# Kernel optimization log

Measured on AMD Instinct MI355X. Metric: run time of the kernel, lower is better.

The kernel has to match this reference:

```python
import jax, jax.numpy as jnp
import numpy as np

K = 8          # number of nearest neighbors (init kwarg k)
EPS = 1e-16    # torch_geometric clamps squared distance at 1e-16


def setup_inputs() -> dict:
    key = jax.random.key(0)
    k1, k2, k3, k4 = jax.random.split(key, 4)
    N, D, B = 16384, 128, 64
    x1 = jax.random.normal(k1, (N, 3 + D), dtype=jnp.float32)  # true graph: [coords(3) | feats(D)]
    x2 = jax.random.normal(k2, (N, 3 + D), dtype=jnp.float32)  # pred graph
    b1 = jnp.sort(jax.random.randint(k3, (N,), 0, B))          # sorted per-node graph ids
    b2 = jnp.sort(jax.random.randint(k4, (N,), 0, B))
    return {"x1": x1, "x2": x2, "b1": b1, "b2": b2}


def _knn_interpolate(f1, c1, c2, b1, b2, k):
    # Squared pairwise distances [N2, N1] via ||a||^2 + ||b||^2 - 2ab (GEMM form).
    d2 = (jnp.sum(c2 * c2, axis=-1)[:, None]
          + jnp.sum(c1 * c1, axis=-1)[None, :]
          - 2.0 * (c2 @ c1.T))
    d2 = jnp.maximum(d2, 0.0)
    # Batch-aware kNN: forbid cross-graph neighbors.
    d2 = jnp.where(b2[:, None] != b1[None, :], jnp.inf, d2)
    neg_d2, idx = jax.lax.top_k(-d2, k)          # k smallest distances per target node
    w = 1.0 / jnp.clip(-neg_d2, EPS)             # [N2, k] inverse-squared-distance weights
    nbr = f1[idx]                                # [N2, k, D] gather of neighbor features
    return jnp.einsum('nk,nkd->nd', w, nbr) / jnp.sum(w, axis=-1, keepdims=True)


def reference(x1, x2, b1, b2):
    c1, f1 = x1[:, :3], x1[:, 3:]
    c2, f2 = x2[:, :3], x2[:, 3:]
    f1_interp = _knn_interpolate(f1, c1, c2, b1, b2, K)
    return jnp.mean((f1_interp - f2) ** 2)
```

## Files before the change

kernel.cpp:

```cpp
#include <hip/hip_runtime.h>
#include <math.h>

#define KNN 8
#define QPB 32
#define SUB 16
#define BLK 512
#define CAP 1024

__launch_bounds__(BLK, 4)
__global__ void knn_one(const float* __restrict__ x1,
                        const float* __restrict__ x2,
                        const int* __restrict__ b1,
                        const int* __restrict__ b2,
                        int N, int ROW, float scale,
                        unsigned long long* __restrict__ slot,
                        float* __restrict__ out) {
  __shared__ float4 c4[CAP];
  __shared__ int   bs[CAP];
  __shared__ int   s_info[2];
  __shared__ float wred[BLK / 64];

  const int nwg = (int)gridDim.x;
  const int xcd = (int)blockIdx.x & 7, pos = (int)blockIdx.x >> 3;
  const int q8 = nwg >> 3, r8 = nwg & 7;
  const int bid = (xcd < r8) ? xcd * (q8 + 1) + pos
                             : r8 * (q8 + 1) + (xcd - r8) * q8 + pos;

  const int tid  = threadIdx.x;
  const int lane = tid & 63;
  const int wv   = tid >> 6;
  const int qi   = tid >> 4;
  const int sub  = tid & (SUB - 1);
  const int q0   = bid * QPB;
  const int q    = min(q0 + qi, N - 1);
  const int qlast = min(q0 + QPB - 1, N - 1);

  float qx, qy, qz; int mybatch;
  float f2v[KNN];
  {
    const float* c2 = x2 + (size_t)q * ROW;
    qx = c2[0]; qy = c2[1]; qz = c2[2];
    mybatch = b2[q];
    const float* f2 = c2 + 3 + sub;
#pragma unroll
    for (int t = 0; t < KNN; ++t) f2v[t] = f2[16 * t];
  }
  const float n2 = qx * qx + qy * qy + qz * qz;

  if (wv < 2) {
    const int bb = (wv == 0) ? b2[q0] : b2[qlast];
    const int target = bb + wv;
    int lo = 0, hi = N;
    while (lo < hi) {
      int step = (hi - lo + 63) >> 6;
      int p = lo + lane * step;
      bool pred = (p < hi) && (b1[p] < target);
      int c = __popcll(__ballot(pred));
      if (c == 0) { hi = lo; break; }
      int nlo = lo + (c - 1) * step + 1;
      hi = min(hi, lo + c * step);
      lo = nlo;
    }
    if (lane == 0) s_info[wv] = lo;
  }

  float dist[KNN]; int nidx[KNN];
#pragma unroll
  for (int k = 0; k < KNN; ++k) { dist[k] = INFINITY; nidx[k] = 0; }

  __syncthreads();
  const int s1v = s_info[0], e1v = s_info[1];

  for (int t0 = s1v; t0 < e1v; t0 += CAP) {
    const int t1 = min(t0 + CAP, e1v);
    __syncthreads();
    for (int i = t0 + tid; i < t1; i += BLK) {
      const float* p = x1 + (size_t)i * ROW;
      float cx = p[0], cy = p[1], cz = p[2];
      c4[i - t0] = make_float4(cx, cy, cz, cx * cx + cy * cy + cz * cz);
      bs[i - t0] = b1[i];
    }
    __syncthreads();
    for (int j = t0 + sub; j < t1; j += SUB) {
      float4 c = c4[j - t0];
      int bv = bs[j - t0];
      float d = fmaxf(fmaf(-2.0f, fmaf(qx, c.x, fmaf(qy, c.y, qz * c.z)), n2 + c.w), 0.0f);
      d = (bv == mybatch) ? d : INFINITY;
      bool lt[KNN];
#pragma unroll
      for (int k = 0; k < KNN; ++k) lt[k] = d < dist[k];
#pragma unroll
      for (int k = KNN - 1; k > 0; --k) {
        dist[k] = lt[k - 1] ? dist[k - 1] : (lt[k] ? d : dist[k]);
        nidx[k] = lt[k - 1] ? nidx[k - 1] : (lt[k] ? j : nidx[k]);
      }
      dist[0] = lt[0] ? d : dist[0];
      nidx[0] = lt[0] ? j : nidx[0];
    }
  }

  float acc[KNN];
#pragma unroll
  for (int t = 0; t < KNN; ++t) acc[t] = 0.f;
  float sw = 0.f;
  const float* x1f = x1 + 3 + sub;
#pragma unroll
  for (int r = 0; r < KNN; ++r) {
    float hd = dist[0]; int hx = nidx[0];
    float bd = hd; int bi = hx;
#pragma unroll
    for (int m = 1; m <= 8; m <<= 1) {
      float od = __shfl_xor(bd, m); int oi = __shfl_xor(bi, m);
      if (od < bd || (od == bd && oi < bi)) { bd = od; bi = oi; }
    }
    if (hd == bd && hx == bi) {
#pragma unroll
      for (int k = 0; k < KNN - 1; ++k) { dist[k] = dist[k + 1]; nidx[k] = nidx[k + 1]; }
      dist[KNN - 1] = INFINITY; nidx[KNN - 1] = 0;
    }
    float w = 1.0f / fmaxf(bd, 1e-16f);
    sw += w;
    const float* f = x1f + (size_t)bi * ROW;
#pragma unroll
    for (int t = 0; t < KNN; ++t) acc[t] = fmaf(w, f[16 * t], acc[t]);
  }

  float pacc = 0.0f;
  if (q0 + qi < N) {
    float rinv = 1.0f / sw;
#pragma unroll
    for (int t = 0; t < KNN; ++t) {
      float e = fmaf(acc[t], rinv, -f2v[t]);
      pacc += e * e;
    }
  }
#pragma unroll
  for (int off = 32; off > 0; off >>= 1) pacc += __shfl_xor(pacc, off);
  if (lane == 0) wred[wv] = pacc;
  __syncthreads();

  if (tid == 0) {
    float s = 0.0f;
#pragma unroll
    for (int w = 0; w < BLK / 64; ++w) s += wred[w];
    unsigned long long v =
        ((unsigned long long)(0x5A000000u | (unsigned)bid) << 32) |
        (unsigned long long)__float_as_uint(s);
    __hip_atomic_store(&slot[bid], v, __ATOMIC_RELAXED,
                       __HIP_MEMORY_SCOPE_AGENT);
  }

  if (bid == 0 && wv == 0) {
    const int nblk = nwg;
    float s = 0.0f;
    for (int r = 0; r * 64 + lane < nblk; ++r) {
      int i = r * 64 + lane;
      unsigned tag = 0x5A000000u | (unsigned)i;
      unsigned long long x = __hip_atomic_load(&slot[i], __ATOMIC_RELAXED,
                                               __HIP_MEMORY_SCOPE_AGENT);
      while ((unsigned)(x >> 32) != tag) {
        __builtin_amdgcn_s_sleep(8);
        x = __hip_atomic_load(&slot[i], __ATOMIC_RELAXED,
                              __HIP_MEMORY_SCOPE_AGENT);
      }
      s += __uint_as_float((unsigned)x);
    }
#pragma unroll
    for (int off = 32; off > 0; off >>= 1) s += __shfl_xor(s, off);
    if (lane == 0) out[0] = s * scale;
  }
}

extern "C" void kernel_launch(void* const* d_in, const int* in_sizes, int n_in,
                              void* d_out, int out_size, void* d_ws, size_t ws_size,
                              hipStream_t stream) {
  const float* x1 = (const float*)d_in[0];
  const float* x2 = (const float*)d_in[1];
  const int* b1 = (const int*)d_in[2];
  const int* b2 = (const int*)d_in[3];
  int N = in_sizes[2];
  int ROW = in_sizes[0] / N;
  float* out = (float*)d_out;

  int blocks = (N + QPB - 1) / QPB;
  unsigned long long* slot = (unsigned long long*)d_ws;
  if (ws_size < (size_t)blocks * sizeof(unsigned long long)) return;

  float scale = 1.0f / ((float)N * (float)(ROW - 3));
  knn_one<<<blocks, BLK, 0, stream>>>(x1, x2, b1, b2, N, ROW, scale, slot, out);
}
```

Baseline: 24.64 us.

## Double-buffer candidate tiles and pack distance/index into 64-bit sort keys

Candidate coordinates are now staged through two shared-memory buffers, so the global loads for the next tile are issued while the current tile is scanned. This trades one of the two barriers per tile for a register-held prefetch, with a smaller tile. Distance is computed directly as a squared difference rather than the norm-expansion form. Distance bits and index are packed into one 64-bit key so the top-k insert and the cross-lane merge compare single values, at the cost of 64-bit compares and selects.

```diff
diff --git a/kernel.cpp b/kernel.cpp
--- a/kernel.cpp
+++ b/kernel.cpp
@@ -5,7 +5,7 @@
 #define QPB 32
 #define SUB 16
 #define BLK 512
-#define CAP 1024
+#define CAP 512
 
 __launch_bounds__(BLK, 4)
 __global__ void knn_one(const float* __restrict__ x1,
@@ -15,8 +15,8 @@
                         int N, int ROW, float scale,
                         unsigned long long* __restrict__ slot,
                         float* __restrict__ out) {
-  __shared__ float4 c4[CAP];
-  __shared__ int   bs[CAP];
+  __shared__ float4 c4[2][CAP];
+  __shared__ int   bs[2][CAP];
   __shared__ int   s_info[2];
   __shared__ float wred[BLK / 64];
 
@@ -45,7 +45,6 @@
 #pragma unroll
     for (int t = 0; t < KNN; ++t) f2v[t] = f2[16 * t];
   }
-  const float n2 = qx * qx + qy * qy + qz * qz;
 
   if (wv < 2) {
     const int bb = (wv == 0) ? b2[q0] : b2[qlast];
@@ -64,39 +63,57 @@
     if (lane == 0) s_info[wv] = lo;
   }
 
-  float dist[KNN]; int nidx[KNN];
-#pragma unroll
-  for (int k = 0; k < KNN; ++k) { dist[k] = INFINITY; nidx[k] = 0; }
+  unsigned long long K[KNN];
+  const unsigned long long KINIT = 0x7F800000ULL << 32;
+#pragma unroll
+  for (int k = 0; k < KNN; ++k) K[k] = KINIT;
 
   __syncthreads();
   const int s1v = s_info[0], e1v = s_info[1];
 
-  for (int t0 = s1v; t0 < e1v; t0 += CAP) {
-    const int t1 = min(t0 + CAP, e1v);
+  int t0 = s1v, t1 = min(t0 + CAP, e1v), buf = 0;
+  {
+    int i = t0 + tid;
+    if (i < t1) {
+      const float* p = x1 + (size_t)i * ROW;
+      c4[0][i - t0] = make_float4(p[0], p[1], p[2], 0.f);
+      bs[0][i - t0] = b1[i];
+    }
+  }
+  __syncthreads();
+
+  while (true) {
+    const int tn0 = t1, tn1 = min(tn0 + CAP, e1v);
+    float nx = 0.f, ny = 0.f, nz = 0.f; int nb = 0;
+    const bool have_next = tn0 < e1v;
+    const int ni = tn0 + tid;
+    if (have_next && ni < tn1) {
+      const float* p = x1 + (size_t)ni * ROW;
+      nx = p[0]; ny = p[1]; nz = p[2]; nb = b1[ni];
+    }
+    for (int j = t0 + sub; j < t1; j += SUB) {
+      float4 c = c4[buf][j - t0];
+      int bv = bs[buf][j - t0];
+      float dx = qx - c.x, dy = qy - c.y, dz = qz - c.z;
+      float d = fmaf(dx, dx, fmaf(dy, dy, dz * dz));
+      unsigned long long key =
+          ((unsigned long long)__float_as_uint(d) << 32) | (unsigned)j;
+      key = (bv == mybatch) ? key : ~0ULL;
+      bool lt[KNN];
+#pragma unroll
+      for (int k = 0; k < KNN; ++k) lt[k] = key < K[k];
+#pragma unroll
+      for (int k = KNN - 1; k > 0; --k)
+        K[k] = lt[k - 1] ? K[k - 1] : (lt[k] ? key : K[k]);
+      K[0] = lt[0] ? key : K[0];
+    }
+    if (!have_next) break;
+    if (ni < tn1) {
+      c4[buf ^ 1][ni - tn0] = make_float4(nx, ny, nz, 0.f);
+      bs[buf ^ 1][ni - tn0] = nb;
+    }
     __syncthreads();
-    for (int i = t0 + tid; i < t1; i += BLK) {
-      const float* p = x1 + (size_t)i * ROW;
-      float cx = p[0], cy = p[1], cz = p[2];
-      c4[i - t0] = make_float4(cx, cy, cz, cx * cx + cy * cy + cz * cz);
-      bs[i - t0] = b1[i];
-    }
-    __syncthreads();
-    for (int j = t0 + sub; j < t1; j += SUB) {
-      float4 c = c4[j - t0];
-      int bv = bs[j - t0];
-      float d = fmaxf(fmaf(-2.0f, fmaf(qx, c.x, fmaf(qy, c.y, qz * c.z)), n2 + c.w), 0.0f);
-      d = (bv == mybatch) ? d : INFINITY;
-      bool lt[KNN];
-#pragma unroll
-      for (int k = 0; k < KNN; ++k) lt[k] = d < dist[k];
-#pragma unroll
-      for (int k = KNN - 1; k > 0; --k) {
-        dist[k] = lt[k - 1] ? dist[k - 1] : (lt[k] ? d : dist[k]);
-        nidx[k] = lt[k - 1] ? nidx[k - 1] : (lt[k] ? j : nidx[k]);
-      }
-      dist[0] = lt[0] ? d : dist[0];
-      nidx[0] = lt[0] ? j : nidx[0];
-    }
+    t0 = tn0; t1 = tn1; buf ^= 1;
   }
 
   float acc[KNN];
@@ -106,18 +123,19 @@
   const float* x1f = x1 + 3 + sub;
 #pragma unroll
   for (int r = 0; r < KNN; ++r) {
-    float hd = dist[0]; int hx = nidx[0];
-    float bd = hd; int bi = hx;
+    unsigned long long h = K[0], b = h;
 #pragma unroll
     for (int m = 1; m <= 8; m <<= 1) {
-      float od = __shfl_xor(bd, m); int oi = __shfl_xor(bi, m);
-      if (od < bd || (od == bd && oi < bi)) { bd = od; bi = oi; }
-    }
-    if (hd == bd && hx == bi) {
-#pragma unroll
-      for (int k = 0; k < KNN - 1; ++k) { dist[k] = dist[k + 1]; nidx[k] = nidx[k + 1]; }
-      dist[KNN - 1] = INFINITY; nidx[KNN - 1] = 0;
-    }
+      unsigned long long o = __shfl_xor(b, m);
+      b = (o < b) ? o : b;
+    }
+    if (h == b) {
+#pragma unroll
+      for (int k = 0; k < KNN - 1; ++k) K[k] = K[k + 1];
+      K[KNN - 1] = KINIT;
+    }
+    float bd = __uint_as_float((unsigned)(b >> 32));
+    int   bi = (int)(unsigned)b;
     float w = 1.0f / fmaxf(bd, 1e-16f);
     sw += w;
     const float* f = x1f + (size_t)bi * ROW;
@@ -151,9 +169,8 @@
   }
 
   if (bid == 0 && wv == 0) {
-    const int nblk = nwg;
     float s = 0.0f;
-    for (int r = 0; r * 64 + lane < nblk; ++r) {
+    for (int r = 0; r * 64 + lane < nwg; ++r) {
       int i = r * 64 + lane;
       unsigned tag = 0x5A000000u | (unsigned)i;
       unsigned long long x = __hip_atomic_load(&slot[i], __ATOMIC_RELAXED,
```

Result: slower. 25.17 us (+2.2%).
